# Optimization experiments

Measured on AMD Instinct MI355X. Metric: run time of the kernel, lower is better.

Reference implementation:

```python
import jax, jax.numpy as jnp
import numpy as np

MULT = 4
HIDDEN = 4096
HC_DIM = MULT * HIDDEN              # 16384
MIX_HC = (2 + MULT) * MULT          # 24 = n (pre) + n (post) + n*n (res)
NORM_EPS = 1e-6
SINK_EPS = 1e-6
POST_MULT = 1.0
SINK_ITERS = 10
B = 4096


def setup_inputs() -> dict:
    key = jax.random.key(0)
    k = jax.random.split(key, 7)
    return {
        "x_prev": jax.random.normal(k[0], (B, HIDDEN), jnp.float32),
        "residual_prev": jax.random.normal(k[1], (B, MULT, HIDDEN), jnp.float32),
        "post_mix_prev": jax.random.uniform(k[2], (B, MULT), jnp.float32),
        "comb_mix_prev": jax.random.uniform(k[3], (B, MULT, MULT), jnp.float32),
        # fn scaled so logits stay O(1) after the hc_dim-wide contraction
        "fn": jax.random.normal(k[4], (MIX_HC, HC_DIM), jnp.float32) * 0.01,
        "base": jax.random.normal(k[5], (MIX_HC,), jnp.float32) * 0.02,
        "scale": jax.random.uniform(k[6], (3,), jnp.float32),
    }


def _post_mapping(x, residual, post_mix, comb_mix):
    # residual_new[b,i,:] = sum_j comb[b,i,j] * residual[b,j,:] + post_mix[b,i] * x[b,:]
    return jnp.einsum('bij,bjh->bih', comb_mix, residual) + post_mix[:, :, None] * x[:, None, :]


def _pre_mapping(residual, fn, base, scale):
    n = MULT
    b = residual.shape[0]
    x_flat = residual.reshape(b, HC_DIM)
    # RMS norm over the full hyper-connection dim
    rms = jnp.sqrt(jnp.mean(x_flat * x_flat, axis=-1, keepdims=True) + NORM_EPS)
    x_norm = x_flat / rms
    logits = jnp.einsum('bd,md->bm', x_norm, fn)  # [B, mix_hc]
    pre = logits[:, :n] * scale[0] + base[:n]
    post = logits[:, n:2 * n] * scale[1] + base[n:2 * n]
    res = logits[:, 2 * n:] * scale[2] + base[2 * n:]
    # H_pre on simplex -> weights combining n streams into layer input
    h_pre = jax.nn.softmax(pre, axis=-1)                       # [B, n]
    post_mix = POST_MULT * jax.nn.sigmoid(post)[:, :, None]    # [B, n, 1]
    # H_res doubly stochastic via Sinkhorn-Knopp row/col normalization
    m = jnp.exp(res.reshape(b, n, n))
    def body(m, _):
        m = m / (m.sum(axis=-1, keepdims=True) + SINK_EPS)  # row normalize
        m = m / (m.sum(axis=-2, keepdims=True) + SINK_EPS)  # col normalize
        return m, None
    comb_mix, _ = jax.lax.scan(body, m, None, length=SINK_ITERS)
    layer_input = jnp.einsum('bn,bnh->bh', h_pre, residual)
    return post_mix, comb_mix, layer_input


def reference(x_prev, residual_prev, post_mix_prev, comb_mix_prev, fn, base, scale):
    residual_cur = _post_mapping(x_prev, residual_prev, post_mix_prev, comb_mix_prev)
    post_mix_cur, comb_mix_cur, layer_input_cur = _pre_mapping(residual_cur, fn, base, scale)
    return residual_cur, post_mix_cur, comb_mix_cur, layer_input_cur
```

## Files before the change

### kernel.cpp

```cpp
#include <hip/hip_runtime.h>
#include <math.h>

#define HIDDEN 4096
#define MULT 4
#define HCD 16384
#define MIX 24
#define BB 4096

#define KA_THREADS 512
#define ROWS 32
#define HSPLIT 8
#define HSLICE 512
#define TILE_H 64
#define NTILES 8
#define TILE_D 256

#define BAR() asm volatile("s_waitcnt lgkmcnt(0)\n\ts_barrier" ::: "memory")

__global__ __launch_bounds__(256) void k_transpose_fn(const float* __restrict__ fn,
                                                      float* __restrict__ fnT) {
    const int d = blockIdx.x * 256 + threadIdx.x;
    float v[MIX];
#pragma unroll
    for (int m = 0; m < MIX; ++m) v[m] = fn[(size_t)m * HCD + d];
    float4* dst = (float4*)(fnT + (size_t)d * MIX);
#pragma unroll
    for (int m4 = 0; m4 < MIX / 4; ++m4)
        dst[m4] = make_float4(v[4*m4+0], v[4*m4+1], v[4*m4+2], v[4*m4+3]);
}

__global__ __launch_bounds__(KA_THREADS, 8)
void k_main(const float* __restrict__ x_prev, const float* __restrict__ res_prev,
            const float* __restrict__ pm_prev, const float* __restrict__ comb_prev,
            const float* __restrict__ fnT, float* __restrict__ res_cur,
            float* __restrict__ part_lg, float* __restrict__ part_sq)
{
    __shared__ float A[ROWS * TILE_D];
    const int tid  = threadIdx.x;
    const int rg   = blockIdx.x >> 3;
    const int hq   = blockIdx.x & 7;
    const int row1 = tid >> 4;
    const int q    = tid & 15;
    const int b1   = rg * ROWS + row1;
    const int wid  = tid >> 6;
    const int lane = tid & 63;
    const int row2 = lane & 31;
    const int mh   = lane >> 5;

    float comb[MULT][MULT], pm[MULT];
#pragma unroll
    for (int i = 0; i < MULT; ++i) {
        pm[i] = pm_prev[(size_t)b1 * MULT + i];
#pragma unroll
        for (int j = 0; j < MULT; ++j)
            comb[i][j] = comb_prev[(size_t)b1 * 16 + i * 4 + j];
    }

    float acc[MIX];
#pragma unroll
    for (int m = 0; m < MIX; ++m) acc[m] = 0.f;
    float ssq = 0.f;

    const int sw1   = (row1 & 7) << 2;
    const int sw2   = (row2 & 7) << 2;
    const int i_str = wid >> 1;
    const int hoffb = (wid & 1) * 32;

#pragma unroll 1
    for (int t = 0; t < NTILES; ++t) {
        const int h0 = hq * HSLICE + t * TILE_H;
        const size_t gh = (size_t)h0 + q * 4;
        const float4 xv = *(const float4*)(x_prev + (size_t)b1 * HIDDEN + gh);
        float4 rv[MULT];
#pragma unroll
        for (int j = 0; j < MULT; ++j)
            rv[j] = *(const float4*)(res_prev + ((size_t)b1 * MULT + j) * HIDDEN + gh);
#pragma unroll
        for (int i = 0; i < MULT; ++i) {
            float4 r;
            r.x = pm[i] * xv.x; r.y = pm[i] * xv.y;
            r.z = pm[i] * xv.z; r.w = pm[i] * xv.w;
#pragma unroll
            for (int j = 0; j < MULT; ++j) {
                r.x += comb[i][j] * rv[j].x; r.y += comb[i][j] * rv[j].y;
                r.z += comb[i][j] * rv[j].z; r.w += comb[i][j] * rv[j].w;
            }
            *(float4*)(res_cur + ((size_t)b1 * MULT + i) * HIDDEN + gh) = r;
            ssq += r.x*r.x + r.y*r.y + r.z*r.z + r.w*r.w;
            const int dl = i * TILE_H + q * 4;
            *(float4*)(&A[row1 * TILE_D + (dl ^ sw1)]) = r;
        }
        BAR();
#pragma unroll
        for (int k = 0; k < 8; ++k) {
            const int dl = wid * 32 + k * 4;
            const float4 av = *(const float4*)(&A[row2 * TILE_D + (dl ^ sw2)]);
            const int dg = i_str * HIDDEN + h0 + hoffb + k * 4;
            const float* fp = fnT + (size_t)__builtin_amdgcn_readfirstlane(dg) * MIX;
#pragma unroll
            for (int m = 0; m < MIX; ++m) acc[m] += av.x * fp[m];
#pragma unroll
            for (int m = 0; m < MIX; ++m) acc[m] += av.y * fp[MIX + m];
#pragma unroll
            for (int m = 0; m < MIX; ++m) acc[m] += av.z * fp[2 * MIX + m];
#pragma unroll
            for (int m = 0; m < MIX; ++m) acc[m] += av.w * fp[3 * MIX + m];
        }
        BAR();
    }

    ssq += __shfl_down(ssq, 8);
    ssq += __shfl_down(ssq, 4);
    ssq += __shfl_down(ssq, 2);
    ssq += __shfl_down(ssq, 1);
    if (q == 0) part_sq[(size_t)hq * BB + b1] = ssq;

    {
        const int base = (row2 * 8 + wid) * 24 + mh * 12;
        if (mh == 0) {
#pragma unroll
            for (int j4 = 0; j4 < 3; ++j4)
                *(float4*)(&A[base + j4 * 4]) =
                    make_float4(acc[j4*4+0], acc[j4*4+1], acc[j4*4+2], acc[j4*4+3]);
        } else {
#pragma unroll
            for (int j4 = 0; j4 < 3; ++j4)
                *(float4*)(&A[base + j4 * 4]) =
                    make_float4(acc[12+j4*4+0], acc[12+j4*4+1], acc[12+j4*4+2], acc[12+j4*4+3]);
        }
    }
    __syncthreads();
#pragma unroll 1
    for (int it = tid; it < ROWS * MIX; it += KA_THREADS) {
        const int row = it / MIX;
        const int m   = it - row * MIX;
        float s = 0.f;
#pragma unroll
        for (int w = 0; w < 8; ++w) s += A[(row * 8 + w) * 24 + m];
        part_lg[((size_t)hq * BB + rg * ROWS + row) * MIX + m] = s;
    }
}

__global__ __launch_bounds__(256) void k_finalize(
        const float* __restrict__ part_lg, const float* __restrict__ part_sq,
        const float* __restrict__ basep, const float* __restrict__ scale,
        float* __restrict__ post_mix, float* __restrict__ comb_out,
        float* __restrict__ h_pre)
{
    const int row = blockIdx.x * 256 + threadIdx.x;
    float lg[MIX];
#pragma unroll
    for (int m = 0; m < MIX; ++m) lg[m] = 0.f;
    float ssq = 0.f;
#pragma unroll
    for (int w = 0; w < HSPLIT; ++w) {
        const float* p = part_lg + ((size_t)w * BB + row) * MIX;
#pragma unroll
        for (int m = 0; m < MIX; ++m) lg[m] += p[m];
        ssq += part_sq[(size_t)w * BB + row];
    }
    const float rms = sqrtf(ssq * (1.0f / (float)HCD) + 1e-6f);
    const float inv = 1.0f / rms;
    const float s0 = scale[0], s1 = scale[1], s2 = scale[2];

    float pre[4], post[4], rr[16];
#pragma unroll
    for (int i = 0; i < 4; ++i)  pre[i]  = lg[i]     * inv * s0 + basep[i];
#pragma unroll
    for (int i = 0; i < 4; ++i)  post[i] = lg[4 + i] * inv * s1 + basep[4 + i];
#pragma unroll
    for (int k = 0; k < 16; ++k) rr[k]   = lg[8 + k] * inv * s2 + basep[8 + k];

    const float mx = fmaxf(fmaxf(pre[0], pre[1]), fmaxf(pre[2], pre[3]));
    float e[4], es = 0.f;
#pragma unroll
    for (int i = 0; i < 4; ++i) { e[i] = expf(pre[i] - mx); es += e[i]; }
    const float esr = 1.0f / es;
    float4 hp = make_float4(e[0]*esr, e[1]*esr, e[2]*esr, e[3]*esr);
    *(float4*)(h_pre + (size_t)row * 4) = hp;

    float4 pmv = make_float4(1.f/(1.f+expf(-post[0])), 1.f/(1.f+expf(-post[1])),
                             1.f/(1.f+expf(-post[2])), 1.f/(1.f+expf(-post[3])));
    *(float4*)(post_mix + (size_t)row * 4) = pmv;

    float M[16];
#pragma unroll
    for (int k = 0; k < 16; ++k) M[k] = expf(rr[k]);
#pragma unroll 1
    for (int it = 0; it < 10; ++it) {
#pragma unroll
        for (int i = 0; i < 4; ++i) {
            const float rs = 1.0f /
                (M[i*4+0] + M[i*4+1] + M[i*4+2] + M[i*4+3] + 1e-6f);
#pragma unroll
            for (int j = 0; j < 4; ++j) M[i*4+j] *= rs;
        }
#pragma unroll
        for (int j = 0; j < 4; ++j) {
            const float cs = 1.0f /
                (M[j] + M[4+j] + M[8+j] + M[12+j] + 1e-6f);
#pragma unroll
            for (int i = 0; i < 4; ++i) M[i*4+j] *= cs;
        }
    }
#pragma unroll
    for (int m4 = 0; m4 < 4; ++m4)
        *(float4*)(comb_out + (size_t)row * 16 + m4 * 4) =
            make_float4(M[4*m4+0], M[4*m4+1], M[4*m4+2], M[4*m4+3]);
}

__global__ __launch_bounds__(256) void k_layer(const float* __restrict__ res_cur,
                                               const float* __restrict__ h_pre,
                                               float* __restrict__ out)
{
    const int g = blockIdx.x * 256 + threadIdx.x;
    const int b = g >> 10;
    const int c = g & 1023;
    const float4 hp = *(const float4*)(h_pre + (size_t)b * 4);
    const float hpa[4] = {hp.x, hp.y, hp.z, hp.w};
    const float* basep = res_cur + (size_t)b * MULT * HIDDEN + (size_t)c * 4;
    float4 o; o.x = o.y = o.z = o.w = 0.f;
#pragma unroll
    for (int i = 0; i < 4; ++i) {
        const float4 v = *(const float4*)(basep + (size_t)i * HIDDEN);
        o.x += hpa[i]*v.x; o.y += hpa[i]*v.y; o.z += hpa[i]*v.z; o.w += hpa[i]*v.w;
    }
    *(float4*)(out + (size_t)b * HIDDEN + (size_t)c * 4) = o;
}

extern "C" void kernel_launch(void* const* d_in, const int* in_sizes, int n_in,
                              void* d_out, int out_size, void* d_ws, size_t ws_size,
                              hipStream_t stream) {
    const float* x_prev    = (const float*)d_in[0];
    const float* res_prev  = (const float*)d_in[1];
    const float* pm_prev   = (const float*)d_in[2];
    const float* comb_prev = (const float*)d_in[3];
    const float* fn        = (const float*)d_in[4];
    const float* base      = (const float*)d_in[5];
    const float* scale     = (const float*)d_in[6];

    float* out = (float*)d_out;
    float* res_cur  = out;
    float* post_mix = out + 67108864;
    float* comb_out = out + 67108864 + 16384;
    float* layer_in = out + 67108864 + 16384 + 65536;

    float* ws = (float*)d_ws;
    float* fnT     = ws;
    float* part_lg = ws + 393216;
    float* part_sq = ws + 393216 + 786432;
    float* h_pre   = ws + 393216 + 786432 + 32768;

    k_transpose_fn<<<HCD / 256, 256, 0, stream>>>(fn, fnT);
    k_main<<<(BB / ROWS) * HSPLIT, KA_THREADS, 0, stream>>>(
        x_prev, res_prev, pm_prev, comb_prev, fnT, res_cur, part_lg, part_sq);
    k_finalize<<<BB / 256, 256, 0, stream>>>(part_lg, part_sq, base, scale,
                                             post_mix, comb_out, h_pre);
    k_layer<<<(BB * HIDDEN / 4) / 256, 256, 0, stream>>>(res_cur, h_pre, layer_in);
}
```

Measured before the change: 821.7 us.

## Fuse finalize and layer-input kernels into one per-row post kernel

```diff
diff --git a/kernel.cpp b/kernel.cpp
--- a/kernel.cpp
+++ b/kernel.cpp
@@ -29,7 +29,7 @@
         dst[m4] = make_float4(v[4*m4+0], v[4*m4+1], v[4*m4+2], v[4*m4+3]);
 }
 
-__global__ __launch_bounds__(KA_THREADS, 8)
+__global__ __launch_bounds__(KA_THREADS, 4)
 void k_main(const float* __restrict__ x_prev, const float* __restrict__ res_prev,
             const float* __restrict__ pm_prev, const float* __restrict__ comb_prev,
             const float* __restrict__ fnT, float* __restrict__ res_cur,
@@ -129,7 +129,7 @@
                     make_float4(acc[12+j4*4+0], acc[12+j4*4+1], acc[12+j4*4+2], acc[12+j4*4+3]);
         }
     }
-    __syncthreads();
+    BAR();
 #pragma unroll 1
     for (int it = tid; it < ROWS * MIX; it += KA_THREADS) {
         const int row = it / MIX;
@@ -141,91 +141,101 @@
     }
 }
 
-__global__ __launch_bounds__(256) void k_finalize(
+__global__ __launch_bounds__(256) void k_post(
         const float* __restrict__ part_lg, const float* __restrict__ part_sq,
         const float* __restrict__ basep, const float* __restrict__ scale,
+        const float* __restrict__ res_cur,
         float* __restrict__ post_mix, float* __restrict__ comb_out,
-        float* __restrict__ h_pre)
+        float* __restrict__ layer_in)
 {
-    const int row = blockIdx.x * 256 + threadIdx.x;
-    float lg[MIX];
-#pragma unroll
-    for (int m = 0; m < MIX; ++m) lg[m] = 0.f;
-    float ssq = 0.f;
-#pragma unroll
-    for (int w = 0; w < HSPLIT; ++w) {
-        const float* p = part_lg + ((size_t)w * BB + row) * MIX;
-#pragma unroll
-        for (int m = 0; m < MIX; ++m) lg[m] += p[m];
-        ssq += part_sq[(size_t)w * BB + row];
-    }
-    const float rms = sqrtf(ssq * (1.0f / (float)HCD) + 1e-6f);
-    const float inv = 1.0f / rms;
-    const float s0 = scale[0], s1 = scale[1], s2 = scale[2];
-
-    float pre[4], post[4], rr[16];
-#pragma unroll
-    for (int i = 0; i < 4; ++i)  pre[i]  = lg[i]     * inv * s0 + basep[i];
-#pragma unroll
-    for (int i = 0; i < 4; ++i)  post[i] = lg[4 + i] * inv * s1 + basep[4 + i];
-#pragma unroll
-    for (int k = 0; k < 16; ++k) rr[k]   = lg[8 + k] * inv * s2 + basep[8 + k];
-
-    const float mx = fmaxf(fmaxf(pre[0], pre[1]), fmaxf(pre[2], pre[3]));
-    float e[4], es = 0.f;
-#pragma unroll
-    for (int i = 0; i < 4; ++i) { e[i] = expf(pre[i] - mx); es += e[i]; }
-    const float esr = 1.0f / es;
-    float4 hp = make_float4(e[0]*esr, e[1]*esr, e[2]*esr, e[3]*esr);
-    *(float4*)(h_pre + (size_t)row * 4) = hp;
-
-    float4 pmv = make_float4(1.f/(1.f+expf(-post[0])), 1.f/(1.f+expf(-post[1])),
-                             1.f/(1.f+expf(-post[2])), 1.f/(1.f+expf(-post[3])));
-    *(float4*)(post_mix + (size_t)row * 4) = pmv;
-
-    float M[16];
-#pragma unroll
-    for (int k = 0; k < 16; ++k) M[k] = expf(rr[k]);
+    const int b   = blockIdx.x;
+    const int tid = threadIdx.x;
+    __shared__ float red[MIX + 1];
+    __shared__ float hp_s[4];
+
+    if (tid < MIX) {
+        float s = 0.f;
+#pragma unroll
+        for (int w = 0; w < HSPLIT; ++w)
+            s += part_lg[((size_t)w * BB + b) * MIX + tid];
+        red[tid] = s;
+    } else if (tid == MIX) {
+        float s = 0.f;
+#pragma unroll
+        for (int w = 0; w < HSPLIT; ++w) s += part_sq[(size_t)w * BB + b];
+        red[MIX] = s;
+    }
+    __syncthreads();
+
+    if (tid == 0) {
+        const float rms = sqrtf(red[MIX] * (1.0f / (float)HCD) + 1e-6f);
+        const float inv = 1.0f / rms;
+        const float s0 = scale[0], s1 = scale[1], s2 = scale[2];
+
+        float pre[4], post[4], rr[16];
+#pragma unroll
+        for (int i = 0; i < 4; ++i)  pre[i]  = red[i]     * inv * s0 + basep[i];
+#pragma unroll
+        for (int i = 0; i < 4; ++i)  post[i] = red[4 + i] * inv * s1 + basep[4 + i];
+#pragma unroll
+        for (int k = 0; k < 16; ++k) rr[k]   = red[8 + k] * inv * s2 + basep[8 + k];
+
+        const float mx = fmaxf(fmaxf(pre[0], pre[1]), fmaxf(pre[2], pre[3]));
+        float e[4], es = 0.f;
+#pragma unroll
+        for (int i = 0; i < 4; ++i) { e[i] = expf(pre[i] - mx); es += e[i]; }
+        const float esr = 1.0f / es;
+#pragma unroll
+        for (int i = 0; i < 4; ++i) hp_s[i] = e[i] * esr;
+
+        float4 pmv = make_float4(1.f/(1.f+expf(-post[0])), 1.f/(1.f+expf(-post[1])),
+                                 1.f/(1.f+expf(-post[2])), 1.f/(1.f+expf(-post[3])));
+        *(float4*)(post_mix + (size_t)b * 4) = pmv;
+
+        float M[16];
+#pragma unroll
+        for (int k = 0; k < 16; ++k) M[k] = expf(rr[k]);
 #pragma unroll 1
-    for (int it = 0; it < 10; ++it) {
-#pragma unroll
-        for (int i = 0; i < 4; ++i) {
-            const float rs = 1.0f /
-                (M[i*4+0] + M[i*4+1] + M[i*4+2] + M[i*4+3] + 1e-6f);
-#pragma unroll
-            for (int j = 0; j < 4; ++j) M[i*4+j] *= rs;
-        }
-#pragma unroll
-        for (int j = 0; j < 4; ++j) {
-            const float cs = 1.0f /
-                (M[j] + M[4+j] + M[8+j] + M[12+j] + 1e-6f);
-#pragma unroll
-            for (int i = 0; i < 4; ++i) M[i*4+j] *= cs;
-        }
-    }
-#pragma unroll
-    for (int m4 = 0; m4 < 4; ++m4)
-        *(float4*)(comb_out + (size_t)row * 16 + m4 * 4) =
-            make_float4(M[4*m4+0], M[4*m4+1], M[4*m4+2], M[4*m4+3]);
-}
-
-__global__ __launch_bounds__(256) void k_layer(const float* __restrict__ res_cur,
-                                               const float* __restrict__ h_pre,
-                                               float* __restrict__ out)
-{
-    const int g = blockIdx.x * 256 + threadIdx.x;
-    const int b = g >> 10;
-    const int c = g & 1023;
-    const float4 hp = *(const float4*)(h_pre + (size_t)b * 4);
-    const float hpa[4] = {hp.x, hp.y, hp.z, hp.w};
-    const float* basep = res_cur + (size_t)b * MULT * HIDDEN + (size_t)c * 4;
-    float4 o; o.x = o.y = o.z = o.w = 0.f;
-#pragma unroll
-    for (int i = 0; i < 4; ++i) {
-        const float4 v = *(const float4*)(basep + (size_t)i * HIDDEN);
-        o.x += hpa[i]*v.x; o.y += hpa[i]*v.y; o.z += hpa[i]*v.z; o.w += hpa[i]*v.w;
-    }
-    *(float4*)(out + (size_t)b * HIDDEN + (size_t)c * 4) = o;
+        for (int it = 0; it < 10; ++it) {
+#pragma unroll
+            for (int i = 0; i < 4; ++i) {
+                const float rs = 1.0f /
+                    (M[i*4+0] + M[i*4+1] + M[i*4+2] + M[i*4+3] + 1e-6f);
+#pragma unroll
+                for (int j = 0; j < 4; ++j) M[i*4+j] *= rs;
+            }
+#pragma unroll
+            for (int j = 0; j < 4; ++j) {
+                const float cs = 1.0f /
+                    (M[j] + M[4+j] + M[8+j] + M[12+j] + 1e-6f);
+#pragma unroll
+                for (int i = 0; i < 4; ++i) M[i*4+j] *= cs;
+            }
+        }
+#pragma unroll
+        for (int m4 = 0; m4 < 4; ++m4)
+            *(float4*)(comb_out + (size_t)b * 16 + m4 * 4) =
+                make_float4(M[4*m4+0], M[4*m4+1], M[4*m4+2], M[4*m4+3]);
+    }
+    __syncthreads();
+
+    const float h0 = hp_s[0], h1 = hp_s[1], h2 = hp_s[2], h3 = hp_s[3];
+    const float* rp = res_cur + (size_t)b * (MULT * HIDDEN);
+    float* op = layer_in + (size_t)b * HIDDEN;
+#pragma unroll
+    for (int c = 0; c < 4; ++c) {
+        const int c4 = (tid + c * 256) * 4;
+        const float4 v0 = *(const float4*)(rp + 0 * HIDDEN + c4);
+        const float4 v1 = *(const float4*)(rp + 1 * HIDDEN + c4);
+        const float4 v2 = *(const float4*)(rp + 2 * HIDDEN + c4);
+        const float4 v3 = *(const float4*)(rp + 3 * HIDDEN + c4);
+        float4 o;
+        o.x = h0*v0.x + h1*v1.x + h2*v2.x + h3*v3.x;
+        o.y = h0*v0.y + h1*v1.y + h2*v2.y + h3*v3.y;
+        o.z = h0*v0.z + h1*v1.z + h2*v2.z + h3*v3.z;
+        o.w = h0*v0.w + h1*v1.w + h2*v2.w + h3*v3.w;
+        *(float4*)(op + c4) = o;
+    }
 }
 
 extern "C" void kernel_launch(void* const* d_in, const int* in_sizes, int n_in,
@@ -249,12 +259,10 @@
     float* fnT     = ws;
     float* part_lg = ws + 393216;
     float* part_sq = ws + 393216 + 786432;
-    float* h_pre   = ws + 393216 + 786432 + 32768;
 
     k_transpose_fn<<<HCD / 256, 256, 0, stream>>>(fn, fnT);
     k_main<<<(BB / ROWS) * HSPLIT, KA_THREADS, 0, stream>>>(
         x_prev, res_prev, pm_prev, comb_prev, fnT, res_cur, part_lg, part_sq);
-    k_finalize<<<BB / 256, 256, 0, stream>>>(part_lg, part_sq, base, scale,
-                                             post_mix, comb_out, h_pre);
-    k_layer<<<(BB * HIDDEN / 4) / 256, 256, 0, stream>>>(res_cur, h_pre, layer_in);
-}
+    k_post<<<BB, 256, 0, stream>>>(part_lg, part_sq, base, scale, res_cur,
+                                   post_mix, comb_out, layer_in);
+}
```

Result: faster. 675.7 us (-17.8%).
